# Optimization experiments

Measured on AMD Instinct MI355X. Metric: run time of the kernel, lower is better.

## Reference

```python
import jax, jax.numpy as jnp
import numpy as np

B, S, D = 2, 1024, 2048
H, HKV, HD = 16, 8, 128
F, E, R = 5632, 8, 16
EPS = 1e-5
SCALE = 2.0  # lora_alpha / r = 32 / 16


def _rope_tables():
    pos = jnp.arange(S, dtype=jnp.float32)
    inv = 1.0 / (10000.0 ** (jnp.arange(0, HD, 2, dtype=jnp.float32) / HD))
    ang = pos[:, None] * inv[None, :]  # [S, HD/2]
    return jnp.cos(ang), jnp.sin(ang)


def setup_inputs() -> dict:
    key = jax.random.key(0)
    ks = jax.random.split(key, 18)
    p = lambda k, shp: jax.random.normal(k, shp, dtype=jnp.float32) * 0.02
    cos, sin = _rope_tables()
    return {
        'data': jax.random.normal(ks[0], (B, S, D), dtype=jnp.float32),
        'mask': jnp.zeros((1, 1, S, S), dtype=jnp.float32),
        'rope_cos': cos,
        'rope_sin': sin,
        'attn_norm_w': jnp.ones((D,), jnp.float32),
        'ffn_norm_w': jnp.ones((D,), jnp.float32),
        'wq': p(ks[1], (D, D)),
        'wk': p(ks[2], (HKV * HD, D)),
        'wv': p(ks[3], (HKV * HD, D)),
        'wo': p(ks[4], (D, D)),
        'gate_w': p(ks[5], (E, D)),
        'w1': p(ks[6], (F, D)),
        'w2': p(ks[7], (D, F)),
        'w3': p(ks[8], (F, D)),
        'w1_a': p(ks[9], (E, R, D)),
        'w1_b': p(ks[10], (E, F, R)),
        'w3_a': p(ks[11], (E, R, D)),
        'w3_b': p(ks[12], (E, F, R)),
        'w2_a': p(ks[13], (E, R, F)),
        'w2_b': p(ks[14], (E, D, R)),
    }


def _rmsnorm(x, w):
    v = jnp.mean(x.astype(jnp.float32) ** 2, axis=-1, keepdims=True)
    return (x * jax.lax.rsqrt(v + EPS)).astype(x.dtype) * w


def _rope(x, cos, sin):
    # x: [B,S,h,HD]; interleaved-pair rotation (llama apply_rotary_emb)
    x1, x2 = x[..., 0::2], x[..., 1::2]
    c, s = cos[None, :, None, :], sin[None, :, None, :]
    o1 = x1 * c - x2 * s
    o2 = x1 * s + x2 * c
    return jnp.stack([o1, o2], axis=-1).reshape(x.shape)


def reference(data, mask, rope_cos, rope_sin, attn_norm_w, ffn_norm_w,
              wq, wk, wv, wo, gate_w, w1, w2, w3,
              w1_a, w1_b, w3_a, w3_b, w2_a, w2_b):
    # ---- attention block ----
    xn = _rmsnorm(data, attn_norm_w)
    q = (xn @ wq.T).reshape(B, S, H, HD)
    k = (xn @ wk.T).reshape(B, S, HKV, HD)
    v = (xn @ wv.T).reshape(B, S, HKV, HD)
    q = _rope(q, rope_cos, rope_sin)
    k = _rope(k, rope_cos, rope_sin)
    k = jnp.repeat(k, H // HKV, axis=2)  # repeat_kv
    v = jnp.repeat(v, H // HKV, axis=2)
    scores = jnp.einsum('bqhd,bkhd->bhqk', q, k) / np.float32(np.sqrt(HD)) + mask
    probs = jax.nn.softmax(scores, axis=-1)
    attn = jnp.einsum('bhqk,bkhd->bqhd', probs, v).reshape(B, S, H * HD)
    data = data + attn @ wo.T
    # ---- MoE block ----
    sn = _rmsnorm(data, ffn_norm_w)
    logits = sn @ gate_w.T  # [B,S,E]
    # NOTE: source uses F.softmax(..., dim=1) -> softmax over SEQ axis, replicated faithfully
    rw = jax.nn.softmax(logits.astype(jnp.float32), axis=1)
    rw, sel = jax.lax.top_k(rw, 2)  # over experts (last axis)
    rw = rw / jnp.sum(rw, axis=-1, keepdims=True)
    c1 = sn @ w1.T  # [B,S,F]
    c3 = sn @ w3.T
    acc = jnp.zeros_like(data)
    for e in range(E):  # dense per-expert loop, as in source
        h1 = c1 + ((sn @ w1_a[e].T) @ w1_b[e].T) * SCALE
        h3 = c3 + ((sn @ w3_a[e].T) @ w3_b[e].T) * SCALE
        sr = jax.nn.silu(h1) * h3
        h = sr @ w2.T + ((sr @ w2_a[e].T) @ w2_b[e].T) * SCALE
        ew = jnp.sum(rw * (sel == e), axis=-1, keepdims=True).astype(h.dtype)
        acc = acc + h * ew
    return data + acc
```

## Files before the change

kernel.cpp:

```cpp
#include <hip/hip_runtime.h>
#include <hip/hip_bf16.h>
#include <stdint.h>

#define DEVI __device__ __forceinline__

typedef __attribute__((ext_vector_type(8))) short short8;
typedef __attribute__((ext_vector_type(4))) short short4b;
typedef __attribute__((ext_vector_type(4))) float f32x4;

constexpr int Bb  = 2, Ss = 1024, Dd = 2048, Hh = 16, HKVv = 8, HDd = 128;
constexpr int Ff  = 5632, Ee = 8, Rr = 16;
constexpr int Tt  = Bb * Ss;
constexpr int M2  = 2 * Tt;
constexpr int NKV = HKVv * HDd;
constexpr int NQKV = Dd + 2 * NKV;
constexpr int F2  = 2 * Ff;

DEVI unsigned short f2bf(float f) {
  union { float f; unsigned u; } x; x.f = f;
  unsigned r = (x.u + 0x7FFFu + ((x.u >> 16) & 1u)) >> 16;
  return (unsigned short)r;
}
DEVI float bf2f(unsigned short h) {
  union { unsigned u; float f; } x; x.u = ((unsigned)h) << 16; return x.f;
}
DEVI float wsum64(float v) {
  #pragma unroll
  for (int d = 1; d < 64; d <<= 1) v += __shfl_xor(v, d, 64);
  return v;
}
DEVI float wsum16(float v) {
  v += __shfl_xor(v, 1, 64); v += __shfl_xor(v, 2, 64);
  v += __shfl_xor(v, 4, 64); v += __shfl_xor(v, 8, 64);
  return v;
}
DEVI float wmax16(float v) {
  v = fmaxf(v, __shfl_xor(v, 1, 64)); v = fmaxf(v, __shfl_xor(v, 2, 64));
  v = fmaxf(v, __shfl_xor(v, 4, 64)); v = fmaxf(v, __shfl_xor(v, 8, 64));
  return v;
}
typedef __attribute__((address_space(1))) void gvoid;
typedef __attribute__((address_space(3))) void lvoid;
DEVI void gl_lds16(const void* g, void* l) {
  __builtin_amdgcn_global_load_lds((gvoid*)g, (lvoid*)l, 16, 0, 0);
}
DEVI unsigned ldsoff(const void* p) {
  return (unsigned)(uintptr_t)(lvoid*)p;
}
DEVI f32x4 mfma16x16(short8 a, short8 b, f32x4 c) {
  return __builtin_amdgcn_mfma_f32_16x16x32_bf16(a, b, c, 0, 0, 0);
}

__global__ __launch_bounds__(256) void cast_w(const float* __restrict__ in,
                                              unsigned short* __restrict__ out, int n) {
  int i = (blockIdx.x * 256 + threadIdx.x) * 8;
  if (i >= n) return;
  const float4* p = (const float4*)(in + i);
  float4 a = p[0], b = p[1];
  float v[8] = {a.x,a.y,a.z,a.w,b.x,b.y,b.z,b.w};
  short8 o;
  #pragma unroll
  for (int j = 0; j < 8; ++j) o[j] = (short)f2bf(v[j]);
  *(short8*)(out + i) = o;
}
__global__ __launch_bounds__(256) void cast_split_w(const float* __restrict__ in,
                                                    unsigned short* __restrict__ oh,
                                                    unsigned short* __restrict__ ol, int n) {
  int i = (blockIdx.x * 256 + threadIdx.x) * 8;
  if (i >= n) return;
  const float4* p = (const float4*)(in + i);
  float4 a = p[0], b = p[1];
  float v[8] = {a.x,a.y,a.z,a.w,b.x,b.y,b.z,b.w};
  short8 h, l;
  #pragma unroll
  for (int j = 0; j < 8; ++j) {
    unsigned short hb = f2bf(v[j]);
    h[j] = (short)hb;
    l[j] = (short)f2bf(v[j] - bf2f(hb));
  }
  *(short8*)(oh + i) = h;
  *(short8*)(ol + i) = l;
}

__global__ __launch_bounds__(256) void rmsnorm_k(const float* __restrict__ x,
                                                 const float* __restrict__ w,
                                                 unsigned short* __restrict__ out) {
  int row = blockIdx.x, tid = threadIdx.x;
  const float* xr = x + (size_t)row * Dd;
  const float4* p4 = (const float4*)(xr + tid * 8);
  float4 a = p4[0], b = p4[1];
  float v[8] = {a.x,a.y,a.z,a.w,b.x,b.y,b.z,b.w};
  float ss = 0.f;
  #pragma unroll
  for (int j = 0; j < 8; ++j) ss += v[j] * v[j];
  ss = wsum64(ss);
  __shared__ float red[4];
  int wv_ = tid >> 6, l = tid & 63;
  if (l == 0) red[wv_] = ss;
  __syncthreads();
  float tot = red[0] + red[1] + red[2] + red[3];
  float rstd = rsqrtf(tot * (1.0f / Dd) + 1e-5f);
  const float* wr = w + tid * 8;
  short8 o;
  #pragma unroll
  for (int j = 0; j < 8; ++j) o[j] = (short)f2bf(v[j] * rstd * wr[j]);
  *(short8*)(out + (size_t)row * Dd + tid * 8) = o;
}

__global__ __launch_bounds__(256) void rmsnorm_split_k(const float* __restrict__ x,
                                                       const float* __restrict__ w,
                                                       unsigned short* __restrict__ outh,
                                                       unsigned short* __restrict__ outl) {
  int row = blockIdx.x, tid = threadIdx.x;
  const float* xr = x + (size_t)row * Dd;
  const float4* p4 = (const float4*)(xr + tid * 8);
  float4 a = p4[0], b = p4[1];
  float v[8] = {a.x,a.y,a.z,a.w,b.x,b.y,b.z,b.w};
  float ss = 0.f;
  #pragma unroll
  for (int j = 0; j < 8; ++j) ss += v[j] * v[j];
  ss = wsum64(ss);
  __shared__ float red[4];
  int wv_ = tid >> 6, l = tid & 63;
  if (l == 0) red[wv_] = ss;
  __syncthreads();
  float tot = red[0] + red[1] + red[2] + red[3];
  float rstd = rsqrtf(tot * (1.0f / Dd) + 1e-5f);
  const float* wr = w + tid * 8;
  short8 oh, ol;
  #pragma unroll
  for (int j = 0; j < 8; ++j) {
    float val = v[j] * rstd * wr[j];
    unsigned short hb = f2bf(val);
    oh[j] = (short)hb;
    ol[j] = (short)f2bf(val - bf2f(hb));
  }
  *(short8*)(outh + (size_t)row * Dd + tid * 8) = oh;
  *(short8*)(outl + (size_t)row * Dd + tid * 8) = ol;
}

template <int MODE>
__global__ __launch_bounds__(512) void gemm_bt64_v3(const unsigned short* __restrict__ A,
                                                    const unsigned short* __restrict__ Bw,
                                                    void* __restrict__ C0,
                                                    void* __restrict__ C1,
                                                    int M, int N, int Kext, int ld, int gx) {
  __shared__ __align__(16) unsigned short As[128 * 64];
  __shared__ __align__(16) unsigned short Bs[128 * 64];
  int tid = threadIdx.x;
  int w = tid >> 6, l = tid & 63;
  int lr = l & 15, lg = l >> 4;
  int cpx = (int)gridDim.x >> 3;
  int bid = blockIdx.x;
  int swz = (bid & 7) * cpx + (bid >> 3);
  int bx = swz % gx, by = swz / gx;
  int mtiles = M >> 7;
  int ks = 0;
  if (by >= mtiles) { ks = 1; by -= mtiles; }
  int m0 = by * 128, n0 = bx * 128;
  int koff = ks * Kext;
  int wr = (w >> 1) * 32, wc = (w & 1) * 64;
  f32x4 acc[2][4];
  #pragma unroll
  for (int i = 0; i < 2; ++i)
    #pragma unroll
    for (int j = 0; j < 4; ++j) acc[i][j] = (f32x4){0.f, 0.f, 0.f, 0.f};

  int srow = w * 16 + (l >> 3);
  int schunk = (l & 7) ^ (l >> 3);
  const unsigned short* ga = A  + (size_t)(m0 + srow) * ld + koff + schunk * 8;
  const unsigned short* gb = Bw + (size_t)(n0 + srow) * ld + koff + schunk * 8;
  unsigned short* lA = As + w * 1024;
  unsigned short* lB = Bs + w * 1024;

  for (int k0 = 0; k0 < Kext; k0 += 64) {
    #pragma unroll
    for (int c = 0; c < 2; ++c) {
      gl_lds16(ga + k0 + (size_t)(c * 8) * ld, lA + c * 512);
      gl_lds16(gb + k0 + (size_t)(c * 8) * ld, lB + c * 512);
    }
    __syncthreads();
    #pragma unroll
    for (int kk = 0; kk < 2; ++kk) {
      int rc = ((kk * 4 + lg) ^ (lr & 7)) * 8;
      short8 af[2], bfr[4];
      #pragma unroll
      for (int i = 0; i < 2; ++i)
        af[i]  = *(const short8*)(As + (wr + i * 16 + lr) * 64 + rc);
      #pragma unroll
      for (int j = 0; j < 4; ++j)
        bfr[j] = *(const short8*)(Bs + (wc + j * 16 + lr) * 64 + rc);
      #pragma unroll
      for (int i = 0; i < 2; ++i)
        #pragma unroll
        for (int j = 0; j < 4; ++j) acc[i][j] = mfma16x16(af[i], bfr[j], acc[i][j]);
    }
    __syncthreads();
  }
  float* Cf = (float*)(ks ? C1 : C0);
  #pragma unroll
  for (int i = 0; i < 2; ++i)
    #pragma unroll
    for (int j = 0; j < 4; ++j) {
      int m = m0 + wr + i * 16 + lg * 4;
      int n = n0 + wc + j * 16 + lr;
      #pragma unroll
      for (int r = 0; r < 4; ++r) {
        float vv = acc[i][j][r];
        size_t o = (size_t)(m + r) * N + n;
        if (MODE == 0) ((unsigned short*)C0)[o] = f2bf(vv);
        else           Cf[o] = vv;
      }
    }
}

template <int MODE>
__global__ __launch_bounds__(512) void gemm3_v3(const unsigned short* __restrict__ Ah,
                                                const unsigned short* __restrict__ Al,
                                                const unsigned short* __restrict__ Bh1,
                                                const unsigned short* __restrict__ Bl1,
                                                const unsigned short* __restrict__ Bh2,
                                                const unsigned short* __restrict__ Bl2,
                                                const unsigned short* __restrict__ Bh3,
                                                const unsigned short* __restrict__ Bl3,
                                                int nsplit1, int nsplit2,
                                                void* __restrict__ C0,
                                                const float* __restrict__ resid,
                                                int M, int N, int K, int gx) {
  __shared__ __align__(16) unsigned short Ash[128 * 32];
  __shared__ __align__(16) unsigned short Asl[128 * 32];
  __shared__ __align__(16) unsigned short Bsh[128 * 32];
  __shared__ __align__(16) unsigned short Bsl[128 * 32];
  int tid = threadIdx.x;
  int w = tid >> 6, l = tid & 63;
  int lr = l & 15, lg = l >> 4;
  int cpx = (int)gridDim.x >> 3;
  int bid = blockIdx.x;
  int swz = (bid & 7) * cpx + (bid >> 3);
  int bx = swz % gx, by = swz / gx;
  int m0 = by * 128, n0 = bx * 128;
  int wr = (w >> 1) * 32, wc = (w & 1) * 64;

  const unsigned short* Bh; const unsigned short* Bl; int nb;
  if (n0 < nsplit1)      { Bh = Bh1; Bl = Bl1; nb = n0; }
  else if (n0 < nsplit2) { Bh = Bh2; Bl = Bl2; nb = n0 - nsplit1; }
  else                   { Bh = Bh3; Bl = Bl3; nb = n0 - nsplit2; }

  f32x4 acc[2][4];
  #pragma unroll
  for (int i = 0; i < 2; ++i)
    #pragma unroll
    for (int j = 0; j < 4; ++j) acc[i][j] = (f32x4){0.f, 0.f, 0.f, 0.f};

  int srow = w * 16 + (l >> 2);
  int scol = ((l & 3) ^ ((l >> 3) & 3)) * 8;
  const unsigned short* gah = Ah + (size_t)(m0 + srow) * K + scol;
  const unsigned short* gal = Al + (size_t)(m0 + srow) * K + scol;
  const unsigned short* gbh = Bh + (size_t)(nb + srow) * K + scol;
  const unsigned short* gbl = Bl + (size_t)(nb + srow) * K + scol;
  unsigned short* lAh = Ash + w * 512;
  unsigned short* lAl = Asl + w * 512;
  unsigned short* lBh = Bsh + w * 512;
  unsigned short* lBl = Bsl + w * 512;

  for (int k0 = 0; k0 < K; k0 += 32) {
    gl_lds16(gah + k0, lAh);
    gl_lds16(gal + k0, lAl);
    gl_lds16(gbh + k0, lBh);
    gl_lds16(gbl + k0, lBl);
    __syncthreads();
    int rc = (lg ^ ((lr >> 1) & 3)) * 8;
    short8 afh[2], afl[2], bfh[4], bfl[4];
    #pragma unroll
    for (int i = 0; i < 2; ++i) {
      afh[i] = *(const short8*)(Ash + (wr + i * 16 + lr) * 32 + rc);
      afl[i] = *(const short8*)(Asl + (wr + i * 16 + lr) * 32 + rc);
    }
    #pragma unroll
    for (int j = 0; j < 4; ++j) {
      bfh[j] = *(const short8*)(Bsh + (wc + j * 16 + lr) * 32 + rc);
      bfl[j] = *(const short8*)(Bsl + (wc + j * 16 + lr) * 32 + rc);
    }
    #pragma unroll
    for (int i = 0; i < 2; ++i)
      #pragma unroll
      for (int j = 0; j < 4; ++j) {
        acc[i][j] = mfma16x16(afh[i], bfh[j], acc[i][j]);
        acc[i][j] = mfma16x16(afh[i], bfl[j], acc[i][j]);
        acc[i][j] = mfma16x16(afl[i], bfh[j], acc[i][j]);
      }
    __syncthreads();
  }
  #pragma unroll
  for (int i = 0; i < 2; ++i)
    #pragma unroll
    for (int j = 0; j < 4; ++j) {
      int m = m0 + wr + i * 16 + lg * 4;
      int n = n0 + wc + j * 16 + lr;
      #pragma unroll
      for (int r = 0; r < 4; ++r) {
        float vv = acc[i][j][r];
        size_t o = (size_t)(m + r) * N + n;
        if (MODE == 1) ((float*)C0)[o] = vv;
        else           ((float*)C0)[o] = vv + resid[o];
      }
    }
}

__global__ __launch_bounds__(128) void vsplit_k(const float* __restrict__ qkv,
                                                unsigned short* __restrict__ vh,
                                                unsigned short* __restrict__ vl) {
  int row = blockIdx.x;
  int bas = threadIdx.x * 8;
  const float4* p = (const float4*)(qkv + (size_t)row * NQKV + Dd + NKV + bas);
  float4 a = p[0], b = p[1];
  float v[8] = {a.x,a.y,a.z,a.w,b.x,b.y,b.z,b.w};
  short8 h, l;
  #pragma unroll
  for (int j = 0; j < 8; ++j) {
    unsigned short hb = f2bf(v[j]);
    h[j] = (short)hb;
    l[j] = (short)f2bf(v[j] - bf2f(hb));
  }
  size_t o = (size_t)row * NKV + bas;
  *(short8*)(vh + o) = h;
  *(short8*)(vl + o) = l;
}

__global__ void rope_split_k(const float* __restrict__ x, int xstride,
                             const float* __restrict__ cs, const float* __restrict__ sn,
                             unsigned short* __restrict__ oh, unsigned short* __restrict__ ol,
                             int nh) {
  int row = blockIdx.x;
  int s = row & (Ss - 1);
  int nelem = nh * HDd;
  int bas = threadIdx.x * 8;
  if (bas >= nelem) return;
  const float4* px = (const float4*)(x + (size_t)row * xstride + bas);
  float4 a = px[0], b = px[1];
  float vv[8] = {a.x,a.y,a.z,a.w,b.x,b.y,b.z,b.w};
  int d = bas & (HDd - 1);
  const float* cr = cs + s * 64 + (d >> 1);
  const float* sr = sn + s * 64 + (d >> 1);
  short8 hs, ls;
  #pragma unroll
  for (int p = 0; p < 4; ++p) {
    float x1 = vv[2 * p], x2 = vv[2 * p + 1];
    float c = cr[p], si = sr[p];
    float o1 = x1 * c - x2 * si;
    float o2 = x1 * si + x2 * c;
    unsigned short h1 = f2bf(o1), h2 = f2bf(o2);
    hs[2 * p] = (short)h1;      hs[2 * p + 1] = (short)h2;
    ls[2 * p] = (short)f2bf(o1 - bf2f(h1));
    ls[2 * p + 1] = (short)f2bf(o2 - bf2f(h2));
  }
  size_t o = (size_t)row * nelem + bas;
  *(short8*)(oh + o) = hs;
  *(short8*)(ol + o) = ls;
}

__global__ __launch_bounds__(256) void attn3_k(const unsigned short* __restrict__ qh,
                                               const unsigned short* __restrict__ ql,
                                               const unsigned short* __restrict__ kh,
                                               const unsigned short* __restrict__ kl,
                                               const unsigned short* __restrict__ vh,
                                               const unsigned short* __restrict__ vl,
                                               const float* __restrict__ mask,
                                               unsigned short* __restrict__ aoh,
                                               unsigned short* __restrict__ aol) {
  __shared__ __align__(16) unsigned short Ksh[32 * 128], Ksl[32 * 128];
  __shared__ __align__(16) unsigned short VTh[8 * 528], VTl[8 * 528];
  __shared__ __align__(16) unsigned short Plh[4 * 16 * 40], Pll[4 * 16 * 40];
  int tid = threadIdx.x, w = tid >> 6, l = tid & 63;
  int lr = l & 15, lg = l >> 4;
  int b = blockIdx.y >> 4, h = blockIdx.y & 15, hk = h >> 1;
  int q0 = blockIdx.x * 64 + w * 16;

  short8 qfh[4], qfl[4];
  {
    size_t qoff = ((size_t)((b * Ss + q0 + lr) * Hh + h)) * HDd;
    #pragma unroll
    for (int ds = 0; ds < 4; ++ds) {
      qfh[ds] = *(const short8*)(qh + qoff + ds * 32 + lg * 8);
      qfl[ds] = *(const short8*)(ql + qoff + ds * 32 + lg * 8);
    }
  }

  float mreg[4] = {-1e30f, -1e30f, -1e30f, -1e30f};
  float lreg[4] = {0.f, 0.f, 0.f, 0.f};
  f32x4 oacc[8];
  #pragma unroll
  for (int db = 0; db < 8; ++db) oacc[db] = (f32x4){0.f, 0.f, 0.f, 0.f};

  const float sc = 0.08838834764831845f;
  size_t kvbase = ((size_t)(b * Ss) * HKVv + hk) * HDd;
  const unsigned short* kb_h = kh + kvbase;
  const unsigned short* kb_l = kl + kvbase;
  const unsigned short* vb_h = vh + kvbase;
  const unsigned short* vb_l = vl + kvbase;

  int kc1 = (lr ^ lg) * 8;
  int kc2 = (lr ^ (lg + 4)) * 8;
  int vrow_a = w * 8 + ((l & 7) >> 1);
  int vchunk = ((l >> 3) * 2 + (l & 1)) * 8;
  unsigned short* vh1 = VTh + (2 * w) * 528;
  unsigned short* vh2 = VTh + (2 * w + 1) * 528;
  unsigned short* vl1 = VTl + (2 * w) * 528;
  unsigned short* vl2 = VTl + (2 * w + 1) * 528;
  unsigned vtbh = ldsoff(VTh) + (unsigned)lr * 8u;
  unsigned vtbl = ldsoff(VTl) + (unsigned)lr * 8u;

  for (int kv0 = 0; kv0 < Ss; kv0 += 32) {
    int r1 = kv0 + w * 8 + lg;
    gl_lds16(kb_h + (size_t)r1 * NKV + kc1,       Ksh + w * 1024);
    gl_lds16(kb_h + (size_t)(r1 + 4) * NKV + kc2, Ksh + w * 1024 + 512);
    gl_lds16(kb_l + (size_t)r1 * NKV + kc1,       Ksl + w * 1024);
    gl_lds16(kb_l + (size_t)(r1 + 4) * NKV + kc2, Ksl + w * 1024 + 512);
    int vr0 = kv0 + vrow_a;
    gl_lds16(vb_h + (size_t)vr0 * NKV + vchunk,       vh1);
    gl_lds16(vb_h + (size_t)(vr0 + 4) * NKV + vchunk, vh2);
    gl_lds16(vb_l + (size_t)vr0 * NKV + vchunk,       vl1);
    gl_lds16(vb_l + (size_t)(vr0 + 4) * NKV + vchunk, vl2);
    __syncthreads();

    f32x4 s0 = (f32x4){0.f,0.f,0.f,0.f}, s1 = (f32x4){0.f,0.f,0.f,0.f};
    #pragma unroll
    for (int ds = 0; ds < 4; ++ds) {
      int kcol = ((ds * 4 + lg) ^ (lr & 7)) * 8;
      short8 kh0 = *(const short8*)(Ksh + lr * 128 + kcol);
      short8 kh1 = *(const short8*)(Ksh + (16 + lr) * 128 + kcol);
      short8 kl0 = *(const short8*)(Ksl + lr * 128 + kcol);
      short8 kl1 = *(const short8*)(Ksl + (16 + lr) * 128 + kcol);
      s0 = mfma16x16(qfh[ds], kh0, s0);
      s0 = mfma16x16(qfh[ds], kl0, s0);
      s0 = mfma16x16(qfl[ds], kh0, s0);
      s1 = mfma16x16(qfh[ds], kh1, s1);
      s1 = mfma16x16(qfh[ds], kl1, s1);
      s1 = mfma16x16(qfl[ds], kh1, s1);
    }
    const float* mrow = mask + (size_t)(q0 + lg * 4) * Ss + kv0 + lr;
    #pragma unroll
    for (int r = 0; r < 4; ++r) {
      float a0 = s0[r] * sc + mrow[(size_t)r * Ss];
      float a1 = s1[r] * sc + mrow[(size_t)r * Ss + 16];
      float t = wmax16(fmaxf(a0, a1));
      float mn = fmaxf(mreg[r], t);
      float resc = __expf(mreg[r] - mn);
      mreg[r] = mn;
      float e0 = __expf(a0 - mn), e1 = __expf(a1 - mn);
      float ps = wsum16(e0 + e1);
      lreg[r] = lreg[r] * resc + ps;
      #pragma unroll
      for (int db = 0; db < 8; ++db) oacc[db][r] *= resc;
      unsigned short h0 = f2bf(e0), h1 = f2bf(e1);
      unsigned short* prowh = Plh + (w * 16 + lg * 4 + r) * 40;
      unsigned short* prowl = Pll + (w * 16 + lg * 4 + r) * 40;
      prowh[lr] = h0;            prowh[16 + lr] = h1;
      prowl[lr] = f2bf(e0 - bf2f(h0));
      prowl[16 + lr] = f2bf(e1 - bf2f(h1));
    }
    asm volatile("" ::: "memory");
    short8 pfh = *(const short8*)(Plh + (w * 16 + lr) * 40 + lg * 8);
    short8 pfl = *(const short8*)(Pll + (w * 16 + lr) * 40 + lg * 8);

    short4b v4[16];
    #pragma unroll
    for (int db = 0; db < 8; ++db) {
      #pragma unroll
      for (int t = 0; t < 2; ++t) {
        unsigned off = vtbh + (unsigned)((lg * 2 + t) * 1056 + db * 128);
        asm volatile("ds_read_b64_tr_b16 %0, %1" : "=v"(v4[db * 2 + t]) : "v"(off));
      }
    }
    asm volatile("s_waitcnt lgkmcnt(0)" ::: "memory");
    __builtin_amdgcn_sched_barrier(0);
    #pragma unroll
    for (int db = 0; db < 8; ++db) {
      short8 vf;
      vf[0] = v4[db*2][0]; vf[1] = v4[db*2][1]; vf[2] = v4[db*2][2]; vf[3] = v4[db*2][3];
      vf[4] = v4[db*2+1][0]; vf[5] = v4[db*2+1][1]; vf[6] = v4[db*2+1][2]; vf[7] = v4[db*2+1][3];
      oacc[db] = mfma16x16(pfh, vf, oacc[db]);
      oacc[db] = mfma16x16(pfl, vf, oacc[db]);
    }
    #pragma unroll
    for (int db = 0; db < 8; ++db) {
      #pragma unroll
      for (int t = 0; t < 2; ++t) {
        unsigned off = vtbl + (unsigned)((lg * 2 + t) * 1056 + db * 128);
        asm volatile("ds_read_b64_tr_b16 %0, %1" : "=v"(v4[db * 2 + t]) : "v"(off));
      }
    }
    asm volatile("s_waitcnt lgkmcnt(0)" ::: "memory");
    __builtin_amdgcn_sched_barrier(0);
    #pragma unroll
    for (int db = 0; db < 8; ++db) {
      short8 vf;
      vf[0] = v4[db*2][0]; vf[1] = v4[db*2][1]; vf[2] = v4[db*2][2]; vf[3] = v4[db*2][3];
      vf[4] = v4[db*2+1][0]; vf[5] = v4[db*2+1][1]; vf[6] = v4[db*2+1][2]; vf[7] = v4[db*2+1][3];
      oacc[db] = mfma16x16(pfh, vf, oacc[db]);
    }
    __syncthreads();
  }
  float inv[4];
  #pragma unroll
  for (int r = 0; r < 4; ++r) inv[r] = 1.0f / lreg[r];
  size_t obase = ((size_t)((b * Ss + q0 + lg * 4) * Hh + h)) * HDd + lr;
  #pragma unroll
  for (int db = 0; db < 8; ++db)
    #pragma unroll
    for (int r = 0; r < 4; ++r) {
      float val = oacc[db][r] * inv[r];
      unsigned short hb = f2bf(val);
      size_t o = obase + (size_t)r * Hh * HDd + db * 16;
      aoh[o] = hb;
      aol[o] = f2bf(val - bf2f(hb));
    }
}

__global__ __launch_bounds__(256) void router_logits(const float* __restrict__ x2,
                                                     const float* __restrict__ fnw,
                                                     const float* __restrict__ gw,
                                                     float* __restrict__ logits) {
  int wid = (blockIdx.x * 256 + threadIdx.x) >> 6;
  int l = threadIdx.x & 63;
  if (wid >= Tt) return;
  const float* row = x2 + (size_t)wid * Dd;
  float xs[32]; float ss = 0.f;
  #pragma unroll
  for (int c = 0; c < 32; ++c) { float t = row[c * 64 + l]; xs[c] = t; ss += t * t; }
  ss = wsum64(ss);
  float rstd = rsqrtf(ss * (1.0f / Dd) + 1e-5f);
  #pragma unroll
  for (int c = 0; c < 32; ++c) xs[c] *= rstd * fnw[c * 64 + l];
  for (int e = 0; e < 8; ++e) {
    float a = 0.f;
    #pragma unroll
    for (int c = 0; c < 32; ++c) a += xs[c] * gw[(size_t)e * Dd + c * 64 + l];
    a = wsum64(a);
    if (l == 0) logits[wid * 8 + e] = a;
  }
}
__global__ __launch_bounds__(256) void router_colstats(const float* __restrict__ logits,
                                                       float* __restrict__ mz) {
  int b = blockIdx.x >> 3, e = blockIdx.x & 7;
  int tid = threadIdx.x, wv_ = tid >> 6, l = tid & 63;
  __shared__ float red[4];
  float mx = -1e30f;
  for (int s = tid; s < Ss; s += 256) mx = fmaxf(mx, logits[(size_t)(b * Ss + s) * 8 + e]);
  #pragma unroll
  for (int d = 1; d < 64; d <<= 1) mx = fmaxf(mx, __shfl_xor(mx, d, 64));
  if (l == 0) red[wv_] = mx;
  __syncthreads();
  mx = fmaxf(fmaxf(red[0], red[1]), fmaxf(red[2], red[3]));
  __syncthreads();
  float z = 0.f;
  for (int s = tid; s < Ss; s += 256) z += expf(logits[(size_t)(b * Ss + s) * 8 + e] - mx);
  z = wsum64(z);
  if (l == 0) red[wv_] = z;
  __syncthreads();
  if (tid == 0) {
    mz[(b * 8 + e) * 2] = mx;
    mz[(b * 8 + e) * 2 + 1] = red[0] + red[1] + red[2] + red[3];
  }
}
__global__ __launch_bounds__(256) void router_select(const float* __restrict__ logits,
                                                     const float* __restrict__ mz,
                                                     int* __restrict__ sel,
                                                     float* __restrict__ ewt) {
  int t = blockIdx.x * 256 + threadIdx.x;
  if (t >= Tt) return;
  int b = t >> 10;
  float rw[8];
  #pragma unroll
  for (int e = 0; e < 8; ++e)
    rw[e] = expf(logits[(size_t)t * 8 + e] - mz[(b * 8 + e) * 2]) / mz[(b * 8 + e) * 2 + 1];
  int i0 = 0; float b0 = rw[0];
  #pragma unroll
  for (int e = 1; e < 8; ++e) if (rw[e] > b0) { b0 = rw[e]; i0 = e; }
  int i1 = -1; float b1 = -1.f;
  #pragma unroll
  for (int e = 0; e < 8; ++e) if (e != i0 && rw[e] > b1) { b1 = rw[e]; i1 = e; }
  float s = b0 + b1;
  sel[2 * t] = i0; sel[2 * t + 1] = i1;
  ewt[2 * t] = b0 / s; ewt[2 * t + 1] = b1 / s;
}
__global__ void zero_cnt_k(int* cnt) { if (threadIdx.x < 8) cnt[threadIdx.x] = 0; }
__global__ void gather_k(const int* __restrict__ sel, int* cnt, int* list) {
  int i = blockIdx.x * 256 + threadIdx.x;
  if (i >= M2) return;
  int e = sel[i];
  int pos = atomicAdd(cnt + e, 1);
  list[e * Tt + pos] = i;
}

__global__ __launch_bounds__(256) void lora_up_k(const unsigned short* __restrict__ snb,
                                                 const int* __restrict__ sel,
                                                 const float* __restrict__ w1a,
                                                 const float* __restrict__ w3a,
                                                 float* __restrict__ t1, float* __restrict__ t3) {
  int i = (blockIdx.x * 256 + threadIdx.x) >> 6;
  int l = threadIdx.x & 63;
  if (i >= M2) return;
  int t = i >> 1, e = sel[i];
  const unsigned short* row = snb + (size_t)t * Dd;
  const float* wa1 = w1a + (size_t)e * Rr * Dd;
  const float* wa3 = w3a + (size_t)e * Rr * Dd;
  float a1[16], a3[16];
  #pragma unroll
  for (int r = 0; r < 16; ++r) { a1[r] = 0.f; a3[r] = 0.f; }
  for (int c0 = 0; c0 < 32; c0 += 8) {
    float xs[8];
    #pragma unroll
    for (int c = 0; c < 8; ++c) xs[c] = bf2f(row[(c0 + c) * 64 + l]);
    #pragma unroll
    for (int r = 0; r < 16; ++r) {
      float s1 = a1[r], s3 = a3[r];
      #pragma unroll
      for (int c = 0; c < 8; ++c) {
        s1 += xs[c] * wa1[(size_t)r * Dd + (c0 + c) * 64 + l];
        s3 += xs[c] * wa3[(size_t)r * Dd + (c0 + c) * 64 + l];
      }
      a1[r] = s1; a3[r] = s3;
    }
  }
  #pragma unroll
  for (int r = 0; r < 16; ++r) { a1[r] = wsum64(a1[r]); a3[r] = wsum64(a3[r]); }
  if (l == 0) {
    #pragma unroll
    for (int r = 0; r < 16; ++r) { t1[i * 16 + r] = a1[r]; t3[i * 16 + r] = a3[r]; }
  }
}

__global__ __launch_bounds__(256) void expert_sr_k(const unsigned short* __restrict__ c13,
                                                   const float* __restrict__ t1,
                                                   const float* __restrict__ t3,
                                                   const float* __restrict__ w1b,
                                                   const float* __restrict__ w3b,
                                                   const int* __restrict__ cnt,
                                                   const int* __restrict__ list,
                                                   unsigned short* __restrict__ sr) {
  int e = blockIdx.y;
  int f = blockIdx.x * 256 + threadIdx.x;
  __shared__ float W1[16 * 256], W3[16 * 256];
  #pragma unroll
  for (int r = 0; r < 16; ++r) {
    W1[r * 256 + threadIdx.x] = 2.0f * w1b[((size_t)e * Ff + f) * 16 + r];
    W3[r * 256 + threadIdx.x] = 2.0f * w3b[((size_t)e * Ff + f) * 16 + r];
  }
  __syncthreads();
  int n = cnt[e];
  int chunk = (n + 7) >> 3;
  int pbeg = blockIdx.z * chunk;
  int pend = min(n, pbeg + chunk);
  for (int p = pbeg; p < pend; ++p) {
    int i = list[e * Tt + p];
    int t = i >> 1;
    const float* u1 = t1 + (size_t)i * 16;
    const float* u3 = t3 + (size_t)i * 16;
    float l1 = 0.f, l3 = 0.f;
    #pragma unroll
    for (int r = 0; r < 16; ++r) {
      l1 += u1[r] * W1[r * 256 + threadIdx.x];
      l3 += u3[r] * W3[r * 256 + threadIdx.x];
    }
    float h1 = bf2f(c13[(size_t)t * F2 + f]) + l1;
    float h3 = bf2f(c13[(size_t)t * F2 + Ff + f]) + l3;
    float sv = (h1 / (1.f + __expf(-h1))) * h3;
    sr[(size_t)i * Ff + f] = f2bf(sv);
  }
}

__global__ __launch_bounds__(256) void lora_down_k(const unsigned short* __restrict__ sr,
                                                   const int* __restrict__ sel,
                                                   const float* __restrict__ w2a,
                                                   float* __restrict__ t2) {
  int i = (blockIdx.x * 256 + threadIdx.x) >> 6;
  int l = threadIdx.x & 63;
  if (i >= M2) return;
  int e = sel[i];
  const unsigned short* row = sr + (size_t)i * Ff;
  const float* wa = w2a + (size_t)e * Rr * Ff;
  float acc[16];
  #pragma unroll
  for (int r = 0; r < 16; ++r) acc[r] = 0.f;
  for (int c0 = 0; c0 < 88; c0 += 11) {
    float xs[11];
    #pragma unroll
    for (int c = 0; c < 11; ++c) xs[c] = bf2f(row[(c0 + c) * 64 + l]);
    #pragma unroll
    for (int r = 0; r < 16; ++r) {
      float a = acc[r];
      #pragma unroll
      for (int c = 0; c < 11; ++c) a += xs[c] * wa[(size_t)r * Ff + (c0 + c) * 64 + l];
      acc[r] = a;
    }
  }
  #pragma unroll
  for (int r = 0; r < 16; ++r) acc[r] = wsum64(acc[r]);
  if (l == 0) {
    #pragma unroll
    for (int r = 0; r < 16; ++r) t2[i * 16 + r] = acc[r];
  }
}

__global__ __launch_bounds__(256) void combine_k(const float* __restrict__ hb0,
                                                 const float* __restrict__ hb1,
                                                 const float* __restrict__ t2,
                                                 const int* __restrict__ sel,
                                                 const float* __restrict__ ewt,
                                                 const float* __restrict__ w2b,
                                                 float* __restrict__ out) {
  int t = blockIdx.x;
  int d0 = threadIdx.x * 8;
  int e0 = sel[2 * t], e1 = sel[2 * t + 1];
  float a0 = ewt[2 * t], a1 = ewt[2 * t + 1];
  float uu0[16], uu1[16];
  const float* u0 = t2 + (size_t)(2 * t) * 16;
  const float* u1 = t2 + (size_t)(2 * t + 1) * 16;
  #pragma unroll
  for (int r = 0; r < 16; ++r) { uu0[r] = u0[r]; uu1[r] = u1[r]; }
  const float* wb0 = w2b + (size_t)e0 * Dd * 16;
  const float* wb1 = w2b + (size_t)e1 * Dd * 16;
  size_t r0 = (size_t)(2 * t) * Dd, r1 = (size_t)(2 * t + 1) * Dd;
  float* orow = out + (size_t)t * Dd;
  #pragma unroll
  for (int dd = 0; dd < 8; ++dd) {
    int d = d0 + dd;
    float l0 = 0.f, l1v = 0.f;
    #pragma unroll
    for (int r = 0; r < 16; ++r) {
      l0  += uu0[r] * wb0[(size_t)d * 16 + r];
      l1v += uu1[r] * wb1[(size_t)d * 16 + r];
    }
    float h0 = hb0[r0 + d] + hb1[r0 + d];
    float h1 = hb0[r1 + d] + hb1[r1 + d];
    orow[d] += a0 * (h0 + 2.f * l0) + a1 * (h1 + 2.f * l1v);
  }
}

extern "C" void kernel_launch(void* const* d_in, const int* in_sizes, int n_in,
                              void* d_out, int out_size, void* d_ws, size_t ws_size,
                              hipStream_t stream) {
  const float* data  = (const float*)d_in[0];
  const float* mask  = (const float*)d_in[1];
  const float* ropec = (const float*)d_in[2];
  const float* ropes = (const float*)d_in[3];
  const float* anw   = (const float*)d_in[4];
  const float* fnw   = (const float*)d_in[5];
  const float* wq_f  = (const float*)d_in[6];
  const float* wk_f  = (const float*)d_in[7];
  const float* wv_f  = (const float*)d_in[8];
  const float* wo_f  = (const float*)d_in[9];
  const float* gate  = (const float*)d_in[10];
  const float* w1_f  = (const float*)d_in[11];
  const float* w2_f  = (const float*)d_in[12];
  const float* w3_f  = (const float*)d_in[13];
  const float* w1a   = (const float*)d_in[14];
  const float* w1bl  = (const float*)d_in[15];
  const float* w3a   = (const float*)d_in[16];
  const float* w3bl  = (const float*)d_in[17];
  const float* w2a   = (const float*)d_in[18];
  const float* w2bl  = (const float*)d_in[19];
  float* out = (float*)d_out;

  char* base = (char*)d_ws;
  size_t off = 0;
  auto take = [&](size_t bytes) -> char* {
    char* r = base + off;
    off += (bytes + 255) & ~(size_t)255;
    return r;
  };
  unsigned short* wqh = (unsigned short*)take((size_t)Dd * Dd * 2);
  unsigned short* wql = (unsigned short*)take((size_t)Dd * Dd * 2);
  unsigned short* wkh = (unsigned short*)take((size_t)NKV * Dd * 2);
  unsigned short* wkl = (unsigned short*)take((size_t)NKV * Dd * 2);
  unsigned short* wvh = (unsigned short*)take((size_t)NKV * Dd * 2);
  unsigned short* wvl = (unsigned short*)take((size_t)NKV * Dd * 2);
  unsigned short* woh = (unsigned short*)take((size_t)Dd * Dd * 2);
  unsigned short* wol = (unsigned short*)take((size_t)Dd * Dd * 2);
  unsigned short* w13bf = (unsigned short*)take((size_t)F2 * Dd * 2);
  unsigned short* w2bf  = (unsigned short*)take((size_t)Dd * Ff * 2);
  unsigned short* xh = (unsigned short*)take((size_t)Tt * Dd * 2);
  unsigned short* xl = (unsigned short*)take((size_t)Tt * Dd * 2);
  unsigned short* qhB = (unsigned short*)take((size_t)Tt * Dd * 2);
  unsigned short* qlB = (unsigned short*)take((size_t)Tt * Dd * 2);
  unsigned short* khB = (unsigned short*)take((size_t)Tt * NKV * 2);
  unsigned short* klB = (unsigned short*)take((size_t)Tt * NKV * 2);
  unsigned short* vhB = (unsigned short*)take((size_t)Tt * NKV * 2);
  unsigned short* vlB = (unsigned short*)take((size_t)Tt * NKV * 2);
  unsigned short* srb = (unsigned short*)take((size_t)M2 * Ff * 2);
  float* hb = (float*)take((size_t)M2 * Dd * 4);
  float* t1b = (float*)take((size_t)M2 * 16 * 4);
  float* t3b = (float*)take((size_t)M2 * 16 * 4);
  float* t2b = (float*)take((size_t)M2 * 16 * 4);
  int*   selb = (int*)take((size_t)M2 * 4);
  float* ewtb = (float*)take((size_t)M2 * 4);
  float* logitsb = (float*)take((size_t)Tt * 8 * 4);
  float* mzb = (float*)take((size_t)16 * 2 * 4);
  int*   cntb = (int*)take(8 * 4);
  int*   listb = (int*)take((size_t)8 * Tt * 4);
  if (off > ws_size) return;

  float* qkv = (float*)hb;
  unsigned short* aoh = xh;
  unsigned short* aol = xl;
  unsigned short* snb = qhB;
  unsigned short* c13b = wqh;
  float* hb1 = (float*)xh;

  cast_split_w<<<2048, 256, 0, stream>>>(wq_f, wqh, wql, Dd * Dd);
  cast_split_w<<<1024, 256, 0, stream>>>(wk_f, wkh, wkl, NKV * Dd);
  cast_split_w<<<1024, 256, 0, stream>>>(wv_f, wvh, wvl, NKV * Dd);
  cast_split_w<<<2048, 256, 0, stream>>>(wo_f, woh, wol, Dd * Dd);
  cast_w<<<5632, 256, 0, stream>>>(w1_f, w13bf, Ff * Dd);
  cast_w<<<5632, 256, 0, stream>>>(w3_f, w13bf + (size_t)Ff * Dd, Ff * Dd);
  cast_w<<<5632, 256, 0, stream>>>(w2_f, w2bf, Dd * Ff);

  rmsnorm_split_k<<<Tt, 256, 0, stream>>>(data, anw, xh, xl);
  gemm3_v3<1><<<512, 512, 0, stream>>>(xh, xl, wqh, wql, wkh, wkl, wvh, wvl,
                                       Dd, Dd + NKV, qkv, nullptr, Tt, NQKV, Dd, 32);
  vsplit_k<<<Tt, 128, 0, stream>>>(qkv, vhB, vlB);
  rope_split_k<<<Tt, 256, 0, stream>>>(qkv, NQKV, ropec, ropes, qhB, qlB, Hh);
  rope_split_k<<<Tt, 128, 0, stream>>>(qkv + Dd, NQKV, ropec, ropes, khB, klB, HKVv);
  attn3_k<<<dim3(16, 32), 256, 0, stream>>>(qhB, qlB, khB, klB, vhB, vlB, mask, aoh, aol);
  gemm3_v3<2><<<256, 512, 0, stream>>>(aoh, aol, woh, wol, woh, wol, woh, wol,
                                       Dd, Dd, d_out, data, Tt, Dd, Dd, 16);

  rmsnorm_k<<<Tt, 256, 0, stream>>>(out, fnw, snb);
  router_logits<<<512, 256, 0, stream>>>(out, fnw, gate, logitsb);
  router_colstats<<<16, 256, 0, stream>>>(logitsb, mzb);
  router_select<<<8, 256, 0, stream>>>(logitsb, mzb, selb, ewtb);
  zero_cnt_k<<<1, 64, 0, stream>>>(cntb);
  gather_k<<<16, 256, 0, stream>>>(selb, cntb, listb);
  gemm_bt64_v3<0><<<1408, 512, 0, stream>>>(snb, w13bf, c13b, nullptr, Tt, F2, Dd, Dd, 88);
  lora_up_k<<<1024, 256, 0, stream>>>(snb, selb, w1a, w3a, t1b, t3b);
  expert_sr_k<<<dim3(22, 8, 8), 256, 0, stream>>>(c13b, t1b, t3b, w1bl, w3bl, cntb, listb, srb);
  lora_down_k<<<1024, 256, 0, stream>>>(srb, selb, w2a, t2b);
  gemm_bt64_v3<1><<<1024, 512, 0, stream>>>(srb, w2bf, hb, hb1, M2, Dd, Ff / 2, Ff, 16);
  combine_k<<<Tt, 256, 0, stream>>>(hb, hb1, t2b, selb, ewtb, w2bl, out);
}
```

Before: 1.008 ms.

## Compute LoRA down-projections with per-expert MFMA tiles and split-K atomics

Replaces the scalar per-row LoRA A-projection kernels (lora_up_k, lora_down_k), which read fp32 adapter weights, with MFMA-based kernels. The new kernels group tokens by expert using the gathered lists, process 16-row tiles, and split K across blocks, accumulating results with atomicAdd. The adapter A weights are cast to bf16 up front, and the t1/t2/t3 buffers are zeroed so the atomics can accumulate. The cost is extra cast and zero launches, atomic traffic, fp32 atomic ordering nondeterminism, and bf16 rounding of the adapter weights.

```diff
diff --git a/kernel.cpp b/kernel.cpp
--- a/kernel.cpp
+++ b/kernel.cpp
@@ -80,6 +80,10 @@
   }
   *(short8*)(oh + i) = h;
   *(short8*)(ol + i) = l;
+}
+__global__ __launch_bounds__(256) void zero_f32(float* __restrict__ p, int n) {
+  int i = blockIdx.x * 256 + threadIdx.x;
+  if (i < n) p[i] = 0.f;
 }
 
 __global__ __launch_bounds__(256) void rmsnorm_k(const float* __restrict__ x,
@@ -593,41 +597,69 @@
   list[e * Tt + pos] = i;
 }
 
-__global__ __launch_bounds__(256) void lora_up_k(const unsigned short* __restrict__ snb,
-                                                 const int* __restrict__ sel,
-                                                 const float* __restrict__ w1a,
-                                                 const float* __restrict__ w3a,
-                                                 float* __restrict__ t1, float* __restrict__ t3) {
-  int i = (blockIdx.x * 256 + threadIdx.x) >> 6;
-  int l = threadIdx.x & 63;
-  if (i >= M2) return;
-  int t = i >> 1, e = sel[i];
-  const unsigned short* row = snb + (size_t)t * Dd;
-  const float* wa1 = w1a + (size_t)e * Rr * Dd;
-  const float* wa3 = w3a + (size_t)e * Rr * Dd;
-  float a1[16], a3[16];
-  #pragma unroll
-  for (int r = 0; r < 16; ++r) { a1[r] = 0.f; a3[r] = 0.f; }
-  for (int c0 = 0; c0 < 32; c0 += 8) {
-    float xs[8];
-    #pragma unroll
-    for (int c = 0; c < 8; ++c) xs[c] = bf2f(row[(c0 + c) * 64 + l]);
-    #pragma unroll
-    for (int r = 0; r < 16; ++r) {
-      float s1 = a1[r], s3 = a3[r];
-      #pragma unroll
-      for (int c = 0; c < 8; ++c) {
-        s1 += xs[c] * wa1[(size_t)r * Dd + (c0 + c) * 64 + l];
-        s3 += xs[c] * wa3[(size_t)r * Dd + (c0 + c) * 64 + l];
-      }
-      a1[r] = s1; a3[r] = s3;
-    }
-  }
-  #pragma unroll
-  for (int r = 0; r < 16; ++r) { a1[r] = wsum64(a1[r]); a3[r] = wsum64(a3[r]); }
-  if (l == 0) {
-    #pragma unroll
-    for (int r = 0; r < 16; ++r) { t1[i * 16 + r] = a1[r]; t3[i * 16 + r] = a3[r]; }
+__global__ __launch_bounds__(64) void lora_up_m(const unsigned short* __restrict__ snb,
+                                                const unsigned short* __restrict__ w1ab,
+                                                const unsigned short* __restrict__ w3ab,
+                                                const int* __restrict__ cnt,
+                                                const int* __restrict__ list,
+                                                float* __restrict__ t1,
+                                                float* __restrict__ t3) {
+  int tile = blockIdx.x, e = blockIdx.y, ks = blockIdx.z;
+  int ni = cnt[e];
+  if (tile * 16 >= ni) return;
+  int l = threadIdx.x, lr = l & 15, lg = l >> 4;
+  int slotA = tile * 16 + lr; if (slotA >= ni) slotA = ni - 1;
+  int iA = list[e * Tt + slotA];
+  const unsigned short* arow = snb + (size_t)(iA >> 1) * Dd + ks * 1024;
+  const unsigned short* b1 = w1ab + ((size_t)e * 16 + lr) * Dd + ks * 1024;
+  const unsigned short* b3 = w3ab + ((size_t)e * 16 + lr) * Dd + ks * 1024;
+  f32x4 a1 = (f32x4){0.f,0.f,0.f,0.f}, a3 = (f32x4){0.f,0.f,0.f,0.f};
+  #pragma unroll 4
+  for (int k0 = 0; k0 < 1024; k0 += 32) {
+    short8 af  = *(const short8*)(arow + k0 + lg * 8);
+    short8 b1f = *(const short8*)(b1 + k0 + lg * 8);
+    short8 b3f = *(const short8*)(b3 + k0 + lg * 8);
+    a1 = mfma16x16(af, b1f, a1);
+    a3 = mfma16x16(af, b3f, a3);
+  }
+  #pragma unroll
+  for (int r = 0; r < 4; ++r) {
+    int slot = tile * 16 + lg * 4 + r;
+    if (slot < ni) {
+      int i = list[e * Tt + slot];
+      atomicAdd(&t1[(size_t)i * 16 + lr], a1[r]);
+      atomicAdd(&t3[(size_t)i * 16 + lr], a3[r]);
+    }
+  }
+}
+
+__global__ __launch_bounds__(64) void lora_down_m(const unsigned short* __restrict__ sr,
+                                                  const unsigned short* __restrict__ w2ab,
+                                                  const int* __restrict__ cnt,
+                                                  const int* __restrict__ list,
+                                                  float* __restrict__ t2) {
+  int tile = blockIdx.x, e = blockIdx.y, ks = blockIdx.z;
+  int ni = cnt[e];
+  if (tile * 16 >= ni) return;
+  int l = threadIdx.x, lr = l & 15, lg = l >> 4;
+  int slotA = tile * 16 + lr; if (slotA >= ni) slotA = ni - 1;
+  int iA = list[e * Tt + slotA];
+  const unsigned short* arow = sr + (size_t)iA * Ff + ks * 1408;
+  const unsigned short* brow = w2ab + ((size_t)e * 16 + lr) * Ff + ks * 1408;
+  f32x4 acc = (f32x4){0.f,0.f,0.f,0.f};
+  #pragma unroll 4
+  for (int k0 = 0; k0 < 1408; k0 += 32) {
+    short8 af = *(const short8*)(arow + k0 + lg * 8);
+    short8 bf = *(const short8*)(brow + k0 + lg * 8);
+    acc = mfma16x16(af, bf, acc);
+  }
+  #pragma unroll
+  for (int r = 0; r < 4; ++r) {
+    int slot = tile * 16 + lg * 4 + r;
+    if (slot < ni) {
+      int i = list[e * Tt + slot];
+      atomicAdd(&t2[(size_t)i * 16 + lr], acc[r]);
+    }
   }
 }
 
@@ -667,39 +699,6 @@
     float h3 = bf2f(c13[(size_t)t * F2 + Ff + f]) + l3;
     float sv = (h1 / (1.f + __expf(-h1))) * h3;
     sr[(size_t)i * Ff + f] = f2bf(sv);
-  }
-}
-
-__global__ __launch_bounds__(256) void lora_down_k(const unsigned short* __restrict__ sr,
-                                                   const int* __restrict__ sel,
-                                                   const float* __restrict__ w2a,
-                                                   float* __restrict__ t2) {
-  int i = (blockIdx.x * 256 + threadIdx.x) >> 6;
-  int l = threadIdx.x & 63;
-  if (i >= M2) return;
-  int e = sel[i];
-  const unsigned short* row = sr + (size_t)i * Ff;
-  const float* wa = w2a + (size_t)e * Rr * Ff;
-  float acc[16];
-  #pragma unroll
-  for (int r = 0; r < 16; ++r) acc[r] = 0.f;
-  for (int c0 = 0; c0 < 88; c0 += 11) {
-    float xs[11];
-    #pragma unroll
-    for (int c = 0; c < 11; ++c) xs[c] = bf2f(row[(c0 + c) * 64 + l]);
-    #pragma unroll
-    for (int r = 0; r < 16; ++r) {
-      float a = acc[r];
-      #pragma unroll
-      for (int c = 0; c < 11; ++c) a += xs[c] * wa[(size_t)r * Ff + (c0 + c) * 64 + l];
-      acc[r] = a;
-    }
-  }
-  #pragma unroll
-  for (int r = 0; r < 16; ++r) acc[r] = wsum64(acc[r]);
-  if (l == 0) {
-    #pragma unroll
-    for (int r = 0; r < 16; ++r) t2[i * 16 + r] = acc[r];
   }
 }
 
@@ -799,6 +798,9 @@
   float* mzb = (float*)take((size_t)16 * 2 * 4);
   int*   cntb = (int*)take(8 * 4);
   int*   listb = (int*)take((size_t)8 * Tt * 4);
+  unsigned short* w1ab = (unsigned short*)take((size_t)Ee * Rr * Dd * 2);
+  unsigned short* w3ab = (unsigned short*)take((size_t)Ee * Rr * Dd * 2);
+  unsigned short* w2ab = (unsigned short*)take((size_t)Ee * Rr * Ff * 2);
   if (off > ws_size) return;
 
   float* qkv = (float*)hb;
@@ -815,6 +817,10 @@
   cast_w<<<5632, 256, 0, stream>>>(w1_f, w13bf, Ff * Dd);
   cast_w<<<5632, 256, 0, stream>>>(w3_f, w13bf + (size_t)Ff * Dd, Ff * Dd);
   cast_w<<<5632, 256, 0, stream>>>(w2_f, w2bf, Dd * Ff);
+  cast_w<<<128, 256, 0, stream>>>(w1a, w1ab, Ee * Rr * Dd);
+  cast_w<<<128, 256, 0, stream>>>(w3a, w3ab, Ee * Rr * Dd);
+  cast_w<<<352, 256, 0, stream>>>(w2a, w2ab, Ee * Rr * Ff);
+  zero_f32<<<768, 256, 0, stream>>>(t1b, 3 * M2 * 16);
 
   rmsnorm_split_k<<<Tt, 256, 0, stream>>>(data, anw, xh, xl);
   gemm3_v3<1><<<512, 512, 0, stream>>>(xh, xl, wqh, wql, wkh, wkl, wvh, wvl,
@@ -833,9 +839,9 @@
   zero_cnt_k<<<1, 64, 0, stream>>>(cntb);
   gather_k<<<16, 256, 0, stream>>>(selb, cntb, listb);
   gemm_bt64_v3<0><<<1408, 512, 0, stream>>>(snb, w13bf, c13b, nullptr, Tt, F2, Dd, Dd, 88);
-  lora_up_k<<<1024, 256, 0, stream>>>(snb, selb, w1a, w3a, t1b, t3b);
+  lora_up_m<<<dim3(128, 8, 2), 64, 0, stream>>>(snb, w1ab, w3ab, cntb, listb, t1b, t3b);
   expert_sr_k<<<dim3(22, 8, 8), 256, 0, stream>>>(c13b, t1b, t3b, w1bl, w3bl, cntb, listb, srb);
-  lora_down_k<<<1024, 256, 0, stream>>>(srb, selb, w2a, t2b);
+  lora_down_m<<<dim3(128, 8, 4), 64, 0, stream>>>(srb, w2ab, cntb, listb, t2b);
   gemm_bt64_v3<1><<<1024, 512, 0, stream>>>(srb, w2bf, hb, hb1, M2, Dd, Ff / 2, Ff, 16);
   combine_k<<<Tt, 256, 0, stream>>>(hb, hb1, t2b, selb, ewtb, w2bl, out);
 }
```

Measured after the change: 892.1 us. 11.5% less time.
